# Kernel optimization log

Measured on AMD Instinct MI355X. Metric: run time of the kernel, lower is better.

## Reference

```python
import jax, jax.numpy as jnp
import numpy as np

D = 512
H = 8
DK = D // H
EXP = 2
EPS = 1e-5


def _layernorm(x, g, b):
    mu = jnp.mean(x, axis=-1, keepdims=True)
    var = jnp.mean(jnp.square(x - mu), axis=-1, keepdims=True)
    return (x - mu) * jax.lax.rsqrt(var + EPS) * g + b


def setup_inputs() -> dict:
    key = jax.random.key(0)
    ks = jax.random.split(key, 10)
    B, C = 4, 2048
    s = 0.02
    return {
        "h": jax.random.normal(ks[0], (B, C, D), jnp.float32),
        "adj_bias": jax.random.normal(ks[1], (B, C, C), jnp.float32),
        "w_qkv": jax.random.normal(ks[2], (D, 3 * D), jnp.float32) * s,
        "b_qkv": jnp.zeros((3 * D,), jnp.float32),
        "w_out": jax.random.normal(ks[3], (D, D), jnp.float32) * s,
        "b_out": jnp.zeros((D,), jnp.float32),
        "ln1_g": jnp.ones((D,), jnp.float32),
        "ln1_b": jnp.zeros((D,), jnp.float32),
        "ln2_g": jnp.ones((D,), jnp.float32),
        "ln2_b": jnp.zeros((D,), jnp.float32),
        "w1": jax.random.normal(ks[4], (D, D * EXP), jnp.float32) * s,
        "b1": jnp.zeros((D * EXP,), jnp.float32),
        "w2": jax.random.normal(ks[5], (D * EXP, D), jnp.float32) * s,
        "b2": jnp.zeros((D,), jnp.float32),
    }


def reference(h, adj_bias, w_qkv, b_qkv, w_out, b_out, ln1_g, ln1_b, ln2_g, ln2_b, w1, b1, w2, b2):
    B, C, _ = h.shape
    scale = DK ** -0.5
    h_n = _layernorm(h, ln1_g, ln1_b)
    qkv = (h_n @ w_qkv + b_qkv).reshape(B, C, 3, H, DK)
    q, k, v = (qkv[:, :, i].transpose(0, 2, 1, 3) for i in range(3))  # (B,H,C,DK)
    logits = jnp.einsum('bhqd,bhkd->bhqk', q, k) * scale + adj_bias[:, None, :, :]
    attn = jax.nn.softmax(logits, axis=-1)  # (B,H,C,C); dropout off (eval)
    out = jnp.einsum('bhqk,bhkd->bhqd', attn, v).transpose(0, 2, 1, 3).reshape(B, C, D)
    h = h + out @ w_out + b_out
    ff = _layernorm(h, ln2_g, ln2_b)
    ff = jax.nn.gelu(ff @ w1 + b1, approximate=False) @ w2 + b2
    return h + ff
```

## Files before the change

kernel.cpp:

```cpp
#include <hip/hip_runtime.h>
#include <hip/hip_bf16.h>

#define BDIM 4
#define CDIM 2048
#define DDIM 512
#define HH   8
#define DKH  64
#define NROW (BDIM * CDIM)


typedef unsigned short u16;
typedef unsigned int   u32;
typedef u16   u16x4  __attribute__((ext_vector_type(4)));
typedef u16   u16x8  __attribute__((ext_vector_type(8)));
typedef u32   u32x4  __attribute__((ext_vector_type(4)));
typedef __bf16 bf16x8 __attribute__((ext_vector_type(8)));
typedef __bf16 bf16x2 __attribute__((ext_vector_type(2)));
typedef float f32x4  __attribute__((ext_vector_type(4)));
typedef float f32x16 __attribute__((ext_vector_type(16)));

#define LOG2E 1.4426950408889634f

#define MEMFENCE asm volatile("" ::: "memory")
__device__ __forceinline__ void sbar() {
  MEMFENCE; __builtin_amdgcn_s_barrier(); MEMFENCE;
}
#define VMWAIT(N) asm volatile("s_waitcnt vmcnt(" #N ")" ::: "memory")

__device__ __forceinline__ u16 f2bf(float f) {
  union { float f; unsigned u; } x; x.f = f;
  unsigned u = x.u;
  u += 0x7fffu + ((u >> 16) & 1u);
  return (u16)(u >> 16);
}
__device__ __forceinline__ float bf2f(u16 u) {
  return __builtin_bit_cast(float, (u32)u << 16);
}
__device__ __forceinline__ u32 pk2(float a, float b) {
  bf16x2 t; t[0] = (__bf16)a; t[1] = (__bf16)b;
  return __builtin_bit_cast(u32, t);
}
__device__ __forceinline__ float fexp2(float x) {
  float r;
  asm("v_exp_f32 %0, %1" : "=v"(r) : "v"(x));
  return r;
}

__device__ __forceinline__ void gload_lds16(const u16* gp, u16* lp) {
  __builtin_amdgcn_global_load_lds((__attribute__((address_space(1))) const void*)gp,
                                   (__attribute__((address_space(3))) void*)lp, 16, 0, 0);
}

__device__ __forceinline__ void ln_body(int bx, int tid,
                                        const float* __restrict__ x,
                                        const float* __restrict__ gamma,
                                        const float* __restrict__ beta,
                                        u16* __restrict__ y) {
  int gw = (bx * 256 + tid) >> 6;
  int l  = tid & 63;
  const float* xr = x + (size_t)gw * DDIM;
  float4 a = *(const float4*)(xr + l * 8);
  float4 b = *(const float4*)(xr + l * 8 + 4);
  float s = a.x + a.y + a.z + a.w + b.x + b.y + b.z + b.w;
  float q = a.x*a.x + a.y*a.y + a.z*a.z + a.w*a.w + b.x*b.x + b.y*b.y + b.z*b.z + b.w*b.w;
#pragma unroll
  for (int m = 1; m < 64; m <<= 1) { s += __shfl_xor(s, m); q += __shfl_xor(q, m); }
  float mu  = s * (1.0f / DDIM);
  float var = q * (1.0f / DDIM) - mu * mu;
  float rs  = rsqrtf(var + 1e-5f);
  float4 g0 = *(const float4*)(gamma + l * 8);
  float4 g1 = *(const float4*)(gamma + l * 8 + 4);
  float4 b0 = *(const float4*)(beta + l * 8);
  float4 b1 = *(const float4*)(beta + l * 8 + 4);
  u16x8 o;
  o[0] = f2bf((a.x - mu) * rs * g0.x + b0.x);
  o[1] = f2bf((a.y - mu) * rs * g0.y + b0.y);
  o[2] = f2bf((a.z - mu) * rs * g0.z + b0.z);
  o[3] = f2bf((a.w - mu) * rs * g0.w + b0.w);
  o[4] = f2bf((b.x - mu) * rs * g1.x + b1.x);
  o[5] = f2bf((b.y - mu) * rs * g1.y + b1.y);
  o[6] = f2bf((b.z - mu) * rs * g1.z + b1.z);
  o[7] = f2bf((b.w - mu) * rs * g1.w + b1.w);
  *(u16x8*)(y + (size_t)gw * DDIM + l * 8) = o;
}

__global__ __launch_bounds__(256) void ln_kernel(const float* __restrict__ x,
                                                 const float* __restrict__ gamma,
                                                 const float* __restrict__ beta,
                                                 u16* __restrict__ y) {
  ln_body(blockIdx.x, threadIdx.x, x, gamma, beta, y);
}

__device__ __forceinline__ void adj_body(int f, int t,
                                         const float* __restrict__ adj,
                                         u16* __restrict__ adjC) {
  const int b = f >> 8, kt = (f >> 3) & 31;
  const int q0 = (f & 7) * 256;
  const int ch = t & 7, c16 = ch & 3, hi2 = ch >> 2, m = c16 >> 1;
  const int K0 = m * 32 + ((c16 * 2) & 3) * 8 + hi2 * 4;
#pragma unroll
  for (int itq = 0; itq < 8; ++itq) {
    int q = q0 + itq * 32 + (t >> 3);
    const float* src = adj + ((size_t)b * CDIM + q) * CDIM + kt * 64;
    f32x4 v0 = *(const f32x4*)(src + K0);
    f32x4 v1 = *(const f32x4*)(src + K0 + 8);
    u16x8 o;
    o[0] = f2bf(v0[0] * LOG2E); o[1] = f2bf(v0[1] * LOG2E);
    o[2] = f2bf(v0[2] * LOG2E); o[3] = f2bf(v0[3] * LOG2E);
    o[4] = f2bf(v1[0] * LOG2E); o[5] = f2bf(v1[1] * LOG2E);
    o[6] = f2bf(v1[2] * LOG2E); o[7] = f2bf(v1[3] * LOG2E);
    *(u16x8*)(adjC + ((size_t)(b * 32 + kt) * 2048 + q) * 64 + ch * 8) = o;
  }
}

__global__ __launch_bounds__(256) void setup_kernel(const float* __restrict__ h,
                                                    const float* __restrict__ ln1g,
                                                    const float* __restrict__ ln1b,
                                                    u16* __restrict__ hn,
                                                    const float* __restrict__ wqkv,
                                                    const float* __restrict__ wout,
                                                    const float* __restrict__ w1,
                                                    const float* __restrict__ w2,
                                                    u16* __restrict__ o_qkv,
                                                    u16* __restrict__ o_out,
                                                    u16* __restrict__ o_w1,
                                                    u16* __restrict__ o_w2) {
  const int bx = blockIdx.x;
  const int t = threadIdx.x;
  if (bx < 2048) {
    ln_body(bx, t, h, ln1g, ln1b, hn);
  } else {
    int idx = (bx - 2048) * 256 + t;
    const float* w; u16* wt; int K, N;
    if (idx < 98304)       { w = wqkv; wt = o_qkv; K = 512;  N = 1536; }
    else if (idx < 131072) { idx -= 98304;  w = wout; wt = o_out; K = 512;  N = 512; }
    else if (idx < 196608) { idx -= 131072; w = w1;   wt = o_w1;  K = 512;  N = 1024; }
    else                   { idx -= 196608; w = w2;   wt = o_w2;  K = 1024; N = 512; }
    int kb = K >> 3;
    int n = idx / kb, k0 = (idx - n * kb) * 8;
    u16x8 o;
#pragma unroll
    for (int j = 0; j < 8; ++j) o[j] = f2bf(w[(size_t)(k0 + j) * N + n]);
    *(u16x8*)(wt + (size_t)n * K + k0) = o;
  }
}

template <int EPI>
__device__ __forceinline__ void gemm_epi(int row, int col, float val, int N,
                                         const float* __restrict__ res,
                                         float* __restrict__ outf,
                                         u16* __restrict__ outb,
                                         u16* __restrict__ outq,
                                         u16* __restrict__ outk,
                                         u16* __restrict__ outv) {
  if constexpr (EPI == 0) {
    int t = col >> 9, hh = (col >> 6) & 7, dk = col & 63;
    int bb = row >> 11, cc = row & 2047;
    if (t == 0) {
      val *= 0.125f * LOG2E;
      outq[(((size_t)bb * HH + hh) * CDIM + cc) * DKH + dk] = f2bf(val);
    } else if (t == 1) {
      outk[(((size_t)bb * HH + hh) * CDIM + cc) * DKH + dk] = f2bf(val);
    } else {
      outv[(((size_t)bb * HH + hh) * DKH + dk) * CDIM + cc] = f2bf(val);
    }
  } else if constexpr (EPI == 1) {
    size_t idx = (size_t)row * N + col;
    outf[idx] = val + res[idx];
  } else {
    float g = 0.5f * val * (1.0f + erff(val * 0.70710678118f));
    outb[(size_t)row * N + col] = f2bf(g);
  }
}

template <int EPI>
__device__ __forceinline__ void gemm128_body(int flat, int nbn, int nwg,
                                             const u16* __restrict__ A,
                                             const u16* __restrict__ Bt,
                                             const float* __restrict__ bias,
                                             const float* __restrict__ res,
                                             float* __restrict__ outf,
                                             u16* __restrict__ outb,
                                             u16* __restrict__ outq,
                                             u16* __restrict__ outk,
                                             u16* __restrict__ outv,
                                             int N, int K) {
  __shared__ u16 As[3][128 * 32];
  __shared__ u16 Bs[3][128 * 32];
  const int tid = threadIdx.x;
  const int w = tid >> 6, l = tid & 63;
  const int l15 = l & 15, l4 = l >> 4;
  const int virt = (flat & 7) * (nwg >> 3) + (flat >> 3);
  const int bn = virt % nbn, bm = virt / nbn;
  const int wr = w >> 1, wc = w & 1;

  f32x4 acc[4][4] = {};

  const int sg = (l & 3) ^ ((l >> 2) & 3);
  const u16* Ag = A  + (size_t)(bm * 128 + w * 32 + (l >> 2)) * K + sg * 8;
  const u16* Bg = Bt + (size_t)(bn * 128 + w * 32 + (l >> 2)) * K + sg * 8;

  auto stage = [&](int buf, int k0) {
    gload_lds16(Ag + k0,                  &As[buf][(w * 32 + 0) * 32]);
    gload_lds16(Ag + (size_t)16 * K + k0, &As[buf][(w * 32 + 16) * 32]);
    gload_lds16(Bg + k0,                  &Bs[buf][(w * 32 + 0) * 32]);
    gload_lds16(Bg + (size_t)16 * K + k0, &Bs[buf][(w * 32 + 16) * 32]);
  };

  const int nk = K >> 5;
  stage(0, 0);
  int bcur = 0, bnxt = 1;
#pragma unroll 1
  for (int i = 0; i < nk; ++i) {
    if (i + 1 < nk) {
      stage(bnxt, (i + 1) * 32);
      VMWAIT(4);
    } else {
      VMWAIT(0);
    }
    sbar();
    const u16* AsC = &As[bcur][0];
    const u16* BsC = &Bs[bcur][0];
    bf16x8 af[4], bf[4];
#pragma unroll
    for (int m = 0; m < 4; ++m)
      af[m] = *(const bf16x8*)(&AsC[(wr * 64 + m * 16 + l15) * 32 + ((l4 ^ (l15 & 3)) * 8)]);
#pragma unroll
    for (int n = 0; n < 4; ++n)
      bf[n] = *(const bf16x8*)(&BsC[(wc * 64 + n * 16 + l15) * 32 + ((l4 ^ (l15 & 3)) * 8)]);
#pragma unroll
    for (int m = 0; m < 4; ++m)
#pragma unroll
      for (int n = 0; n < 4; ++n)
        acc[m][n] = __builtin_amdgcn_mfma_f32_16x16x32_bf16(af[m], bf[n], acc[m][n], 0, 0, 0);
    bcur = bnxt;
    bnxt = bnxt + 1 == 3 ? 0 : bnxt + 1;
  }

#pragma unroll
  for (int m = 0; m < 4; ++m) {
    const int row0 = bm * 128 + wr * 64 + m * 16 + l4 * 4;
#pragma unroll
    for (int n = 0; n < 4; ++n) {
      const int col = bn * 128 + wc * 64 + n * 16 + l15;
      const float bv = bias[col];
#pragma unroll
      for (int r = 0; r < 4; ++r)
        gemm_epi<EPI>(row0 + r, col, acc[m][n][r] + bv, N, res, outf, outb, outq, outk, outv);
    }
  }
}

__global__ __launch_bounds__(256) void qkv_adj_kernel(const u16* __restrict__ A,
                                                      const u16* __restrict__ Bt,
                                                      const float* __restrict__ bias,
                                                      u16* __restrict__ outq,
                                                      u16* __restrict__ outk,
                                                      u16* __restrict__ outv,
                                                      const float* __restrict__ adj,
                                                      u16* __restrict__ adjC) {
  if (blockIdx.x < 768) {
    gemm128_body<0>(blockIdx.x, 12, 768, A, Bt, bias, nullptr,
                    nullptr, nullptr, outq, outk, outv, 3 * DDIM, DDIM);
  } else {
    adj_body(blockIdx.x - 768, threadIdx.x, adj, adjC);
  }
}

template <int EPI>
__global__ __launch_bounds__(256) void gemm128k(const u16* __restrict__ A,
                                                const u16* __restrict__ Bt,
                                                const float* __restrict__ bias,
                                                const float* __restrict__ res,
                                                float* __restrict__ outf,
                                                u16* __restrict__ outb,
                                                int M, int N, int K) {
  gemm128_body<EPI>(blockIdx.x + gridDim.x * blockIdx.y, gridDim.x,
                    gridDim.x * gridDim.y, A, Bt, bias, res,
                    outf, outb, nullptr, nullptr, nullptr, N, K);
}

template <int EPI>
__global__ __launch_bounds__(256) void gemm64(const u16* __restrict__ A,
                                              const u16* __restrict__ Bt,
                                              const float* __restrict__ bias,
                                              const float* __restrict__ res,
                                              float* __restrict__ outf,
                                              u16* __restrict__ outb,
                                              int M, int N, int K) {
  __shared__ u16 As[2][64 * 64];
  __shared__ u16 Bs[2][128 * 64];
  const int tid = threadIdx.x;
  const int w = tid >> 6, l = tid & 63;
  const int l15 = l & 15, l4 = l >> 4, l7 = l15 & 7;
  const int nbn = gridDim.x, nwg = gridDim.x * gridDim.y;
  const int flat = blockIdx.x + nbn * blockIdx.y;
  const int virt = (flat & 7) * (nwg >> 3) + (flat >> 3);
  const int bn = virt % nbn, bm = virt / nbn;

  f32x4 acc[4][2] = {};

  const int sg = (l & 7) ^ (l >> 3);
  const u16* Ag = A  + (size_t)(bm * 64  + w * 16 + (l >> 3)) * K + sg * 8;
  const u16* Bg = Bt + (size_t)(bn * 128 + w * 32 + (l >> 3)) * K + sg * 8;

  auto stage = [&](int buf, int k0) {
    gload_lds16(Ag + k0,                  &As[buf][(w * 16 + 0) * 64]);
    gload_lds16(Ag + (size_t)8 * K + k0,  &As[buf][(w * 16 + 8) * 64]);
    gload_lds16(Bg + k0,                  &Bs[buf][(w * 32 + 0) * 64]);
    gload_lds16(Bg + (size_t)8 * K + k0,  &Bs[buf][(w * 32 + 8) * 64]);
    gload_lds16(Bg + (size_t)16 * K + k0, &Bs[buf][(w * 32 + 16) * 64]);
    gload_lds16(Bg + (size_t)24 * K + k0, &Bs[buf][(w * 32 + 24) * 64]);
  };

  stage(0, 0);
  __syncthreads();
  int cur = 0;
  for (int k0 = 0; k0 < K; k0 += 64) {
    if (k0 + 64 < K) stage(cur ^ 1, k0 + 64);
#pragma unroll
    for (int s = 0; s < 2; ++s) {
      bf16x8 af[4], bf[2];
#pragma unroll
      for (int m = 0; m < 4; ++m)
        af[m] = *(const bf16x8*)(&As[cur][(m * 16 + l15) * 64 + (((s * 4 + l4) ^ l7) * 8)]);
#pragma unroll
      for (int n = 0; n < 2; ++n)
        bf[n] = *(const bf16x8*)(&Bs[cur][(w * 32 + n * 16 + l15) * 64 + (((s * 4 + l4) ^ l7) * 8)]);
#pragma unroll
      for (int m = 0; m < 4; ++m)
#pragma unroll
        for (int n = 0; n < 2; ++n)
          acc[m][n] = __builtin_amdgcn_mfma_f32_16x16x32_bf16(af[m], bf[n], acc[m][n], 0, 0, 0);
    }
    __syncthreads();
    cur ^= 1;
  }

#pragma unroll
  for (int m = 0; m < 4; ++m) {
    const int row0 = bm * 64 + m * 16 + l4 * 4;
#pragma unroll
    for (int n = 0; n < 2; ++n) {
      const int col = bn * 128 + w * 32 + n * 16 + l15;
      const float bv = bias[col];
#pragma unroll
      for (int r = 0; r < 4; ++r)
        gemm_epi<EPI>(row0 + r, col, acc[m][n][r] + bv, N, res, outf, outb,
                      nullptr, nullptr, nullptr);
    }
  }
}

__global__ __launch_bounds__(512, 2) void flash_attn(const u16* __restrict__ Q,
                                                     const u16* __restrict__ Kg,
                                                     const u16* __restrict__ Vt,
                                                     const u16* __restrict__ adjC,
                                                     u16* __restrict__ O) {
  __shared__ u16 Ks[2][2][64 * 64];
  __shared__ u16 Vs[2][2][64 * 64];
  __shared__ float lw[4][32];
  __shared__ float lsx[4][32];
  const int flat = blockIdx.x + 16 * blockIdx.y;
  const int virt = (flat & 7) * 64 + (flat >> 3);
  const int qt = virt & 15;
  const int bh = virt >> 4;
  const int b = bh >> 3, hh = bh & 7;
  const int tid = threadIdx.x;
  const int w = tid >> 6, l = tid & 63;
  const int kh = w >> 2, qg = w & 3;
  const int q32 = l & 31, hi = l >> 5;
  const int qglob = qt * 128 + qg * 32 + q32;

  const u16* Qb = Q  + (size_t)bh * CDIM * DKH;
  const u16* Kb = Kg + (size_t)bh * CDIM * DKH;
  const u16* Vb = Vt + (size_t)bh * DKH * CDIM;

  const int srow = qg * 16 + (l >> 3);
  const int sg   = (l & 7) ^ (l >> 3);
  const u16* Kg0 = Kb + (size_t)(srow + 0) * DKH + sg * 8;
  const u16* Kg1 = Kb + (size_t)(srow + 8) * DKH + sg * 8;
  const u16* Vg0 = Vb + (size_t)(srow + 0) * CDIM + sg * 8;
  const u16* Vg1 = Vb + (size_t)(srow + 8) * CDIM + sg * 8;

  bf16x8 qf[4];
#pragma unroll
  for (int s = 0; s < 4; ++s)
    qf[s] = *(const bf16x8*)(Qb + (size_t)qglob * DKH + s * 16 + hi * 8);

  const u16* adjQ = adjC + ((size_t)(b * 32) * 2048 + qglob) * 64 + hi * 32;

  f32x16 oa[2] = {};
  float lsum = 0.f;

  auto stage = [&](int buf, int ktr) {
    int kta = kh * 16 + ktr;
    gload_lds16(Kg0 + (size_t)kta * 4096, &Ks[kh][buf][(qg * 16 + 0) * 64]);
    gload_lds16(Kg1 + (size_t)kta * 4096, &Ks[kh][buf][(qg * 16 + 8) * 64]);
    gload_lds16(Vg0 + kta * 64, &Vs[kh][buf][(qg * 16 + 0) * 64]);
    gload_lds16(Vg1 + kta * 64, &Vs[kh][buf][(qg * 16 + 8) * 64]);
  };
  auto ajload = [&](u16x8* dst, int ktr) {
    const u16* p = adjQ + (size_t)(kh * 16 + ktr) * 131072;
#pragma unroll
    for (int i = 0; i < 4; ++i) dst[i] = *(const u16x8*)(p + i * 8);
  };
  auto computeQK = [&](const u16* KsB, const u16x8* av, f32x16* sa) {
#pragma unroll
    for (int m = 0; m < 2; ++m)
#pragma unroll
      for (int r = 0; r < 16; ++r)
        sa[m][r] = bf2f(av[m * 2 + (r >> 3)][r & 7]);
    __builtin_amdgcn_s_setprio(1);
#pragma unroll
    for (int s = 0; s < 4; ++s)
#pragma unroll
      for (int m = 0; m < 2; ++m) {
        bf16x8 kf = *(const bf16x8*)(&KsB[(m * 32 + q32) * 64 + (((s * 2 + hi) ^ (q32 & 7)) * 8)]);
        sa[m] = __builtin_amdgcn_mfma_f32_32x32x16_bf16(kf, qf[s], sa[m], 0, 0, 0);
      }
    __builtin_amdgcn_s_setprio(0);
  };
  auto computePV = [&](const u16* VsB, f32x16* sa) {
#pragma unroll
    for (int m = 0; m < 2; ++m)
#pragma unroll
      for (int r = 0; r < 16; ++r) {
        float p = fexp2(sa[m][r]);
        sa[m][r] = p;
        lsum += p;
      }
    bf16x8 af[4];
#pragma unroll
    for (int m = 0; m < 2; ++m)
#pragma unroll
      for (int t2 = 0; t2 < 2; ++t2) {
        u32 w0 = pk2(sa[m][t2 * 8 + 0], sa[m][t2 * 8 + 1]);
        u32 w1 = pk2(sa[m][t2 * 8 + 2], sa[m][t2 * 8 + 3]);
        u32 w2 = pk2(sa[m][t2 * 8 + 4], sa[m][t2 * 8 + 5]);
        u32 w3 = pk2(sa[m][t2 * 8 + 6], sa[m][t2 * 8 + 7]);
        auto r02 = __builtin_amdgcn_permlane32_swap(w0, w2, false, false);
        auto r13 = __builtin_amdgcn_permlane32_swap(w1, w3, false, false);
        u32x4 aw;
        aw[0] = r02[0];
        aw[1] = r13[0];
        aw[2] = r02[1];
        aw[3] = r13[1];
        af[m * 2 + t2] = __builtin_bit_cast(bf16x8, aw);
      }
    __builtin_amdgcn_s_setprio(1);
#pragma unroll
    for (int s = 0; s < 4; ++s)
#pragma unroll
      for (int n = 0; n < 2; ++n) {
        bf16x8 vf = *(const bf16x8*)(&VsB[(n * 32 + q32) * 64 + (((s * 2 + hi) ^ (q32 & 7)) * 8)]);
        oa[n] = __builtin_amdgcn_mfma_f32_32x32x16_bf16(af[s], vf, oa[n], 0, 0, 0);
      }
    __builtin_amdgcn_s_setprio(0);
  };

  u16x8 avA[4], avB[4];
  f32x16 sa[2];
  stage(0, 0);
  ajload(avA, 0);
  __syncthreads();
#pragma unroll 1
  for (int it = 0; it < 8; ++it) {
    int ktr = it * 2;
    stage(1, ktr + 1);
    computeQK(&Ks[kh][0][0], avA, sa);
    ajload(avB, ktr + 1);
    computePV(&Vs[kh][0][0], sa);
    __syncthreads();
    if (ktr + 2 < 16) stage(0, ktr + 2);
    computeQK(&Ks[kh][1][0], avB, sa);
    if (ktr + 2 < 16) ajload(avA, ktr + 2);
    computePV(&Vs[kh][1][0], sa);
    __syncthreads();
  }

  lsum += __shfl_xor(lsum, 32);

  float* cb = (float*)&Vs[0][0][0];
  if (kh == 1) {
#pragma unroll
    for (int n = 0; n < 2; ++n)
#pragma unroll
      for (int r = 0; r < 16; ++r)
        cb[((qg * 2 + n) * 16 + r) * 64 + l] = oa[n][r];
    if (hi == 0) lsx[qg][q32] = lsum;
  }
  __syncthreads();
  if (kh == 0) {
    lsum += lsx[qg][q32];
#pragma unroll
    for (int n = 0; n < 2; ++n)
#pragma unroll
      for (int r = 0; r < 16; ++r)
        oa[n][r] += cb[((qg * 2 + n) * 16 + r) * 64 + l];
    lw[qg][q32] = 1.0f / lsum;
#pragma unroll
    for (int n = 0; n < 2; ++n)
#pragma unroll
      for (int r = 0; r < 16; ++r) {
        int qloc = (r & 3) + 8 * (r >> 2) + 4 * hi;
        int row = qt * 128 + qg * 32 + qloc;
        float val = oa[n][r] * lw[qg][qloc];
        O[((size_t)b * CDIM + row) * DDIM + hh * 64 + n * 32 + q32] = f2bf(val);
      }
  }
}

extern "C" void kernel_launch(void* const* d_in, const int* in_sizes, int n_in,
                              void* d_out, int out_size, void* d_ws, size_t ws_size,
                              hipStream_t stream) {
  const float* h      = (const float*)d_in[0];
  const float* adj    = (const float*)d_in[1];
  const float* w_qkv  = (const float*)d_in[2];
  const float* b_qkv  = (const float*)d_in[3];
  const float* w_out  = (const float*)d_in[4];
  const float* b_out  = (const float*)d_in[5];
  const float* ln1g   = (const float*)d_in[6];
  const float* ln1b   = (const float*)d_in[7];
  const float* ln2g   = (const float*)d_in[8];
  const float* ln2b   = (const float*)d_in[9];
  const float* w1     = (const float*)d_in[10];
  const float* b1     = (const float*)d_in[11];
  const float* w2     = (const float*)d_in[12];
  const float* b2     = (const float*)d_in[13];
  float* out = (float*)d_out;

  char* ws = (char*)d_ws;
  u16* adjC  = (u16*)(ws);
  u16* hn    = (u16*)(ws + 33554432);
  u16* qb    = (u16*)(ws + 41943040);
  u16* kb    = (u16*)(ws + 50331648);
  u16* vt    = (u16*)(ws + 58720256);
  u16* attn  = (u16*)(ws + 67108864);
  u16* wqkvt = (u16*)(ws + 75497472);
  u16* woutt = (u16*)(ws + 77070336);
  u16* w1t   = (u16*)(ws + 77594624);
  u16* w2t   = (u16*)(ws + 78643200);
  u16* ffin  = hn;
  u16* ffmid = qb;

  setup_kernel<<<3072, 256, 0, stream>>>(h, ln1g, ln1b, hn,
                                         w_qkv, w_out, w1, w2,
                                         wqkvt, woutt, w1t, w2t);

  qkv_adj_kernel<<<1792, 256, 0, stream>>>(hn, wqkvt, b_qkv, qb, kb, vt,
                                           adj, adjC);

  flash_attn<<<dim3(16, 32), 512, 0, stream>>>(qb, kb, vt, adjC, attn);

  gemm64<1><<<dim3(4, 128), 256, 0, stream>>>(attn, woutt, b_out, h,
                                              out, nullptr, NROW, DDIM, DDIM);

  ln_kernel<<<2048, 256, 0, stream>>>(out, ln2g, ln2b, ffin);

  gemm128k<2><<<dim3(8, 64), 256, 0, stream>>>(ffin, w1t, b1, nullptr,
                                               nullptr, ffmid, NROW, 2 * DDIM, DDIM);

  gemm64<1><<<dim3(4, 128), 256, 0, stream>>>(ffmid, w2t, b2, out,
                                              out, nullptr, NROW, DDIM, 2 * DDIM);
}
```

Measured before the change: 177.3 us.

## Drop key-split in flash attention; each block handles 256 queries over all keys

The attention kernel previously split each 128-query tile's keys across two groups of four waves and merged partial outputs through shared memory. Now all eight waves own distinct 32-query groups of a 256-query tile and each iterates over the full key range, which halves the grid and removes the cross-wave reduction, extra barrier and LDS merge. Each K/V tile staged in LDS is shared by twice as many queries, cutting K/V global traffic. In exchange the grid has only 256 blocks, which may underfill the GPU's compute units, and each wave's serial loop is twice as long.

```diff
diff --git a/kernel.cpp b/kernel.cpp
--- a/kernel.cpp
+++ b/kernel.cpp
@@ -357,31 +357,27 @@
                                                      const u16* __restrict__ Vt,
                                                      const u16* __restrict__ adjC,
                                                      u16* __restrict__ O) {
-  __shared__ u16 Ks[2][2][64 * 64];
-  __shared__ u16 Vs[2][2][64 * 64];
-  __shared__ float lw[4][32];
-  __shared__ float lsx[4][32];
-  const int flat = blockIdx.x + 16 * blockIdx.y;
-  const int virt = (flat & 7) * 64 + (flat >> 3);
-  const int qt = virt & 15;
-  const int bh = virt >> 4;
+  __shared__ u16 Ks[2][64 * 64];
+  __shared__ u16 Vs[2][64 * 64];
+  const int flat = blockIdx.x + 8 * blockIdx.y;
+  const int virt = (flat & 7) * 32 + (flat >> 3);
+  const int qt = virt & 7;
+  const int bh = virt >> 3;
   const int b = bh >> 3, hh = bh & 7;
   const int tid = threadIdx.x;
   const int w = tid >> 6, l = tid & 63;
-  const int kh = w >> 2, qg = w & 3;
+  const int qg = w;
   const int q32 = l & 31, hi = l >> 5;
-  const int qglob = qt * 128 + qg * 32 + q32;
+  const int qglob = qt * 256 + qg * 32 + q32;
 
   const u16* Qb = Q  + (size_t)bh * CDIM * DKH;
   const u16* Kb = Kg + (size_t)bh * CDIM * DKH;
   const u16* Vb = Vt + (size_t)bh * DKH * CDIM;
 
-  const int srow = qg * 16 + (l >> 3);
+  const int srow = qg * 8 + (l >> 3);
   const int sg   = (l & 7) ^ (l >> 3);
-  const u16* Kg0 = Kb + (size_t)(srow + 0) * DKH + sg * 8;
-  const u16* Kg1 = Kb + (size_t)(srow + 8) * DKH + sg * 8;
-  const u16* Vg0 = Vb + (size_t)(srow + 0) * CDIM + sg * 8;
-  const u16* Vg1 = Vb + (size_t)(srow + 8) * CDIM + sg * 8;
+  const u16* Kg0 = Kb + (size_t)srow * DKH + sg * 8;
+  const u16* Vg0 = Vb + (size_t)srow * CDIM + sg * 8;
 
   bf16x8 qf[4];
 #pragma unroll
@@ -393,15 +389,12 @@
   f32x16 oa[2] = {};
   float lsum = 0.f;
 
-  auto stage = [&](int buf, int ktr) {
-    int kta = kh * 16 + ktr;
-    gload_lds16(Kg0 + (size_t)kta * 4096, &Ks[kh][buf][(qg * 16 + 0) * 64]);
-    gload_lds16(Kg1 + (size_t)kta * 4096, &Ks[kh][buf][(qg * 16 + 8) * 64]);
-    gload_lds16(Vg0 + kta * 64, &Vs[kh][buf][(qg * 16 + 0) * 64]);
-    gload_lds16(Vg1 + kta * 64, &Vs[kh][buf][(qg * 16 + 8) * 64]);
+  auto stage = [&](int buf, int kt) {
+    gload_lds16(Kg0 + (size_t)kt * 4096, &Ks[buf][(qg * 8) * 64]);
+    gload_lds16(Vg0 + kt * 64, &Vs[buf][(qg * 8) * 64]);
   };
-  auto ajload = [&](u16x8* dst, int ktr) {
-    const u16* p = adjQ + (size_t)(kh * 16 + ktr) * 131072;
+  auto ajload = [&](u16x8* dst, int kt) {
+    const u16* p = adjQ + (size_t)kt * 131072;
 #pragma unroll
     for (int i = 0; i < 4; ++i) dst[i] = *(const u16x8*)(p + i * 8);
   };
@@ -465,50 +458,32 @@
   ajload(avA, 0);
   __syncthreads();
 #pragma unroll 1
-  for (int it = 0; it < 8; ++it) {
-    int ktr = it * 2;
-    stage(1, ktr + 1);
-    computeQK(&Ks[kh][0][0], avA, sa);
-    ajload(avB, ktr + 1);
-    computePV(&Vs[kh][0][0], sa);
+  for (int it = 0; it < 16; ++it) {
+    int kt = it * 2;
+    stage(1, kt + 1);
+    computeQK(&Ks[0][0], avA, sa);
+    ajload(avB, kt + 1);
+    computePV(&Vs[0][0], sa);
     __syncthreads();
-    if (ktr + 2 < 16) stage(0, ktr + 2);
-    computeQK(&Ks[kh][1][0], avB, sa);
-    if (ktr + 2 < 16) ajload(avA, ktr + 2);
-    computePV(&Vs[kh][1][0], sa);
+    if (kt + 2 < 32) stage(0, kt + 2);
+    computeQK(&Ks[1][0], avB, sa);
+    if (kt + 2 < 32) ajload(avA, kt + 2);
+    computePV(&Vs[1][0], sa);
     __syncthreads();
   }
 
   lsum += __shfl_xor(lsum, 32);
-
-  float* cb = (float*)&Vs[0][0][0];
-  if (kh == 1) {
-#pragma unroll
-    for (int n = 0; n < 2; ++n)
-#pragma unroll
-      for (int r = 0; r < 16; ++r)
-        cb[((qg * 2 + n) * 16 + r) * 64 + l] = oa[n][r];
-    if (hi == 0) lsx[qg][q32] = lsum;
-  }
-  __syncthreads();
-  if (kh == 0) {
-    lsum += lsx[qg][q32];
-#pragma unroll
-    for (int n = 0; n < 2; ++n)
-#pragma unroll
-      for (int r = 0; r < 16; ++r)
-        oa[n][r] += cb[((qg * 2 + n) * 16 + r) * 64 + l];
-    lw[qg][q32] = 1.0f / lsum;
-#pragma unroll
-    for (int n = 0; n < 2; ++n)
-#pragma unroll
-      for (int r = 0; r < 16; ++r) {
-        int qloc = (r & 3) + 8 * (r >> 2) + 4 * hi;
-        int row = qt * 128 + qg * 32 + qloc;
-        float val = oa[n][r] * lw[qg][qloc];
-        O[((size_t)b * CDIM + row) * DDIM + hh * 64 + n * 32 + q32] = f2bf(val);
-      }
-  }
+  float inv = 1.0f / lsum;
+
+#pragma unroll
+  for (int n = 0; n < 2; ++n)
+#pragma unroll
+    for (int r = 0; r < 16; ++r) {
+      int qloc = (r & 3) + 8 * (r >> 2) + 4 * hi;
+      float invr = __shfl(inv, (l & 32) | qloc);
+      int row = qt * 256 + qg * 32 + qloc;
+      O[((size_t)b * CDIM + row) * DDIM + hh * 64 + n * 32 + q32] = f2bf(oa[n][r] * invr);
+    }
 }
 
 extern "C" void kernel_launch(void* const* d_in, const int* in_sizes, int n_in,
@@ -551,7 +526,7 @@
   qkv_adj_kernel<<<1792, 256, 0, stream>>>(hn, wqkvt, b_qkv, qb, kb, vt,
                                            adj, adjC);
 
-  flash_attn<<<dim3(16, 32), 512, 0, stream>>>(qb, kb, vt, adjC, attn);
+  flash_attn<<<dim3(8, 32), 512, 0, stream>>>(qb, kb, vt, adjC, attn);
 
   gemm64<1><<<dim3(4, 128), 256, 0, stream>>>(attn, woutt, b_out, h,
                                               out, nullptr, NROW, DDIM, DDIM);
```

Measured after the change: 177.5 us. No clear change (+0.1%).
